# Optimization experiments

Measured on AMD Instinct MI355X. Metric: run time of the kernel, lower is better.

The kernel has to match this reference:

```python
import jax, jax.numpy as jnp
import numpy as np

B = 128          # number of graphs in the batch
NM, EM = 100000, 400000    # mol nodes / edges
NP, EP = 200000, 3200000   # protein nodes / edges
DM, DP, OD = 78, 54, 16


def setup_inputs() -> dict:
    key = jax.random.key(0)
    ks = jax.random.split(key, 20)
    def w(k, shape):
        return jax.random.normal(k, shape, jnp.float32) * 0.05
    z = lambda n: jnp.zeros((n,), jnp.float32)
    return {
        "mol_x": jax.random.normal(ks[0], (NM, DM), jnp.float32),
        "mol_edge_index": jax.random.randint(ks[1], (2, EM), 0, NM),
        "mol_batch": jnp.sort(jax.random.randint(ks[2], (NM,), 0, B)),
        "pro_x": jax.random.normal(ks[3], (NP, DP), jnp.float32),
        "pro_edge_index": jax.random.randint(ks[4], (2, EP), 0, NP),
        "pro_batch": jnp.sort(jax.random.randint(ks[5], (NP,), 0, B)),
        "mol_W1": w(ks[6], (256, DM)), "mol_b1": z(256),
        "mol_W2": w(ks[7], (7 * OD, 256)), "mol_b2": z(7 * OD),
        "c1_Wl": w(ks[8], (DP, DP)), "c1_bl": z(DP), "c1_Wr": w(ks[9], (DP, DP)),
        "c2_Wl": w(ks[10], (2 * DP, DP)), "c2_bl": z(2 * DP), "c2_Wr": w(ks[11], (2 * DP, DP)),
        "pro_W1": w(ks[12], (256, 2 * DP)), "pro_b1": z(256),
        "pro_W2": w(ks[13], (9 * OD, 256)), "pro_b2": z(9 * OD),
        "fc1_W": w(ks[14], (1024, 16 * OD)), "fc1_b": z(1024),
        "fc2_W": w(ks[15], (512, 1024)), "fc2_b": z(512),
        "out_W": w(ks[16], (1, 512)), "out_b": z(1),
    }


def _seg_mean(x, seg, n):
    s = jax.ops.segment_sum(x, seg, num_segments=n)
    c = jax.ops.segment_sum(jnp.ones((x.shape[0],), x.dtype), seg, num_segments=n)
    return s / jnp.maximum(c, 1.0)[:, None]


def _sage(x, ei, Wl, bl, Wr):
    # PyG SAGEConv (mean aggr): lin_l(mean_{j->i} x_j) + lin_r(x_i); lin_r has no bias
    agg = _seg_mean(x[ei[0]], ei[1], x.shape[0])
    return agg @ Wl.T + bl + x @ Wr.T


def reference(mol_x, mol_edge_index, mol_batch, pro_x, pro_edge_index, pro_batch,
              mol_W1, mol_b1, mol_W2, mol_b2,
              c1_Wl, c1_bl, c1_Wr, c2_Wl, c2_bl, c2_Wr,
              pro_W1, pro_b1, pro_W2, pro_b2,
              fc1_W, fc1_b, fc2_W, fc2_b, out_W, out_b):
    alpha, degree = 0.05, 4
    # APPNP-style k-hop propagation over the unnormalized COO adjacency:
    # (adj @ h)[i] = sum over edges (row=i, col=j) of h[j]
    row, col = mol_edge_index[0], mol_edge_index[1]
    h = mol_x
    emb = alpha * mol_x
    for _ in range(degree):
        h = jax.ops.segment_sum(h[col], row, num_segments=mol_x.shape[0])
        emb = emb + (1.0 - alpha) * h / degree
    x = _seg_mean(emb, mol_batch, B)            # global mean pool -> [B, 78]
    x = jax.nn.relu(x @ mol_W1.T + mol_b1)
    x = x @ mol_W2.T + mol_b2                   # [B, 112]; dropout is identity at eval

    xt = jax.nn.relu(_sage(pro_x, pro_edge_index, c1_Wl, c1_bl, c1_Wr))
    xt = jax.nn.relu(_sage(xt, pro_edge_index, c2_Wl, c2_bl, c2_Wr))
    xt = _seg_mean(xt, pro_batch, B)            # [B, 108]
    xt = jax.nn.relu(xt @ pro_W1.T + pro_b1)
    xt = xt @ pro_W2.T + pro_b2                 # [B, 144]

    xc = jnp.concatenate([x, xt], axis=1)       # [B, 256]
    xc = jax.nn.relu(xc @ fc1_W.T + fc1_b)
    xc = jax.nn.relu(xc @ fc2_W.T + fc2_b)
    return xc @ out_W.T + out_b                 # [B, 1]
```

## Files before the change

kernel.cpp:

```cpp
#include <hip/hip_runtime.h>

#define K256 __launch_bounds__(256)

constexpr int B = 128;
constexpr int NM = 100000, EM = 400000;
constexpr int NP = 200000, EP = 3200000;
constexpr int DM = 78, DPK = 54, DP2 = 108;
constexpr int XH = 32;
constexpr int XH4 = 16;
constexpr int MH = 48;

__device__ __forceinline__ float b2f(unsigned short u) {
  return __uint_as_float((unsigned int)u << 16);
}
__device__ __forceinline__ unsigned short f2b(float f) {
  unsigned int b = __float_as_uint(f);
  return (unsigned short)((b + 0x7fffu + ((b >> 16) & 1u)) >> 16);
}

template <int SH>
__global__ void K256 k_bhist(const int* __restrict__ dst, int* __restrict__ bhist, int E) {
  __shared__ int lh[512];
  int tid = threadIdx.x;
  for (int t = tid; t < 512; t += 256) lh[t] = 0;
  __syncthreads();
  int c0 = blockIdx.x * 4096;
#pragma unroll
  for (int k = 0; k < 16; k++) {
    int e = c0 + k * 256 + tid;
    if (e < E) atomicAdd(&lh[dst[e] >> SH], 1);
  }
  __syncthreads();
  for (int t = tid; t < 512; t += 256) {
    int c = lh[t];
    if (c) atomicAdd(&bhist[t], c);
  }
}

__global__ void k_scanb(const int* __restrict__ bhist, int* __restrict__ bed,
                        int* __restrict__ bcur, int NB, int E) {
  __shared__ int s[512];
  int tid = threadIdx.x;
  int v = (tid < NB) ? bhist[tid] : 0;
  s[tid] = v;
  __syncthreads();
  for (int off = 1; off < 512; off <<= 1) {
    int t = (tid >= off) ? s[tid - off] : 0;
    __syncthreads();
    s[tid] += t;
    __syncthreads();
  }
  int excl = s[tid] - v;
  if (tid < NB) {
    bed[tid] = excl;
    bcur[tid] = excl;
  }
  if (tid == NB - 1) bed[NB] = E;
}

template <int SH>
__global__ void K256 k_bin(const int* __restrict__ src, const int* __restrict__ dst,
                           int* __restrict__ bcur, int2* __restrict__ binned, int E) {
  __shared__ int lh[512];
  __shared__ int gbase[512];
  int c0 = blockIdx.x * 4096;
  int tid = threadIdx.x;
  for (int t = tid; t < 512; t += 256) lh[t] = 0;
  __syncthreads();
  int r[16], dcache[16];
#pragma unroll
  for (int k = 0; k < 16; k++) {
    int e = c0 + k * 256 + tid;
    if (e < E) {
      int d = dst[e];
      dcache[k] = d;
      r[k] = atomicAdd(&lh[d >> SH], 1);
    }
  }
  __syncthreads();
  for (int b = tid; b < 512; b += 256) {
    int c = lh[b];
    gbase[b] = c ? atomicAdd(&bcur[b], c) : 0;
  }
  __syncthreads();
#pragma unroll
  for (int k = 0; k < 16; k++) {
    int e = c0 + k * 256 + tid;
    if (e < E) {
      int d = dcache[k];
      binned[gbase[d >> SH] + r[k]] = make_int2(src[e], d);
    }
  }
}

template <int SH>
__global__ void K256 k_build(const int2* __restrict__ binned, const int* __restrict__ bed,
                             int* __restrict__ deg, int* __restrict__ starts,
                             int* __restrict__ csr, int N) {
  constexpr int NN = 1 << SH;
  constexpr int P = NN / 256;
  __shared__ int lcnt[NN];
  __shared__ int lpair[256];
  int b = blockIdx.x, base = b << SH, tid = threadIdx.x;
  int nn = min(N - base, NN);
  for (int t = tid; t < NN; t += 256) lcnt[t] = 0;
  __syncthreads();
  int e0 = bed[b], e1 = bed[b + 1];
  for (int e = e0 + tid; e < e1; e += 256) atomicAdd(&lcnt[binned[e].y - base], 1);
  __syncthreads();
  int loc[P];
  int psum = 0;
#pragma unroll
  for (int p = 0; p < P; p++) {
    loc[p] = lcnt[tid * P + p];
    psum += loc[p];
  }
  lpair[tid] = psum;
  __syncthreads();
  for (int off = 1; off < 256; off <<= 1) {
    int t = (tid >= off) ? lpair[tid - off] : 0;
    __syncthreads();
    lpair[tid] += t;
    __syncthreads();
  }
  int run = lpair[tid] - psum;
  __syncthreads();
#pragma unroll
  for (int p = 0; p < P; p++) {
    int i = tid * P + p;
    int st = e0 + run;
    if (i < nn) {
      deg[base + i] = loc[p];
      starts[base + i] = st;
    }
    lcnt[i] = st;
    run += loc[p];
  }
  __syncthreads();
  for (int e = e0 + tid; e < e1; e += 256) {
    int2 sd = binned[e];
    int p = atomicAdd(&lcnt[sd.y - base], 1);
    csr[p] = sd.x;
  }
}

__global__ void K256 k_bstart(const int* __restrict__ batch, int* __restrict__ bstart, int N) {
  int i = blockIdx.x * 256 + threadIdx.x;
  if (i < N) {
    int b = batch[i];
    int pb = (i == 0) ? -1 : batch[i - 1];
    for (int bb = pb + 1; bb <= b; bb++) bstart[bb] = i;
    if (i == N - 1)
      for (int bb = b + 1; bb <= B; bb++) bstart[bb] = N;
  }
}

__global__ void k_inv(const int* __restrict__ bstart, float* __restrict__ inv) {
  int b = threadIdx.x;
  if (b < B) inv[b] = 1.f / fmaxf((float)(bstart[b + 1] - bstart[b]), 1.f);
}

__global__ void K256 k_transT(const float* __restrict__ in, float* __restrict__ out, int R,
                              int C) {
  __shared__ float t[32][33];
  int cb = blockIdx.x * 32, rb = blockIdx.y * 32;
  int tx = threadIdx.x & 31, ty = threadIdx.x >> 5;
  for (int i = ty; i < 32; i += 8) {
    int r = rb + i, c = cb + tx;
    if (r < R && c < C) t[i][tx] = in[(size_t)r * C + c];
  }
  __syncthreads();
  for (int i = ty; i < 32; i += 8) {
    int c = cb + i, r = rb + tx;
    if (r < R && c < C) out[(size_t)c * R + r] = t[tx][i];
  }
}

__global__ void K256 k_prepw(const float* __restrict__ c1Wl, const float* __restrict__ c1Wr,
                             const float* __restrict__ c1bl, const float* __restrict__ c2Wl,
                             const float* __restrict__ c2Wr, float* __restrict__ w1cat,
                             float* __restrict__ bl1c, float* __restrict__ w2cat) {
  int i = blockIdx.x * 256 + threadIdx.x;
  if (i < 108 * 56) {
    int k = i / 56, o = i - k * 56;
    w1cat[i] = (o < 54) ? ((k < 54) ? c1Wl[o * 54 + k] : c1Wr[o * 54 + (k - 54)]) : 0.f;
  }
  if (i < 108 * 108) {
    int k = i / 108, o = i - k * 108;
    w2cat[i] = (k < 54) ? c2Wl[o * 54 + k] : c2Wr[o * 54 + (k - 54)];
  }
  if (i < 56) bl1c[i] = (i < 54) ? c1bl[i] : 0.f;
}

template <int DF2, int XHD>
__global__ void K256 k_castg(const float* __restrict__ x, int sstride,
                             ushort2* __restrict__ xh, int N) {
  int t = blockIdx.x * 256 + threadIdx.x;
  if (t < N * DF2) {
    int n = t / DF2, j = t - n * DF2;
    float2 v = *(const float2*)(x + (size_t)n * sstride + 2 * j);
    xh[(size_t)n * XHD + j] = make_ushort2(f2b(v.x), f2b(v.y));
  }
}

__global__ void K256 k_gatherh(const ushort4* __restrict__ xh4, const int* __restrict__ starts,
                               const int* __restrict__ deg, const int* __restrict__ csr,
                               ushort4* __restrict__ outh4, int N) {
  int wid = (blockIdx.x * 256 + threadIdx.x) >> 6;
  int lane = threadIdx.x & 63;
  if (wid >= N) return;
  int s = starts[wid], d = deg[wid];
  const int* cp = csr + s;
  int quarter = lane >> 4, sl = lane & 15;
  bool act = sl < 14;
  float a0 = 0.f, a1 = 0.f, a2 = 0.f, a3 = 0.f;
  float b0 = 0.f, b1 = 0.f, b2 = 0.f, b3 = 0.f;
  int j = 0;
  for (; j + 8 <= d; j += 8) {
    if (act) {
      ushort4 v = xh4[(size_t)cp[j + quarter] * XH4 + sl];
      ushort4 w = xh4[(size_t)cp[j + 4 + quarter] * XH4 + sl];
      a0 += b2f(v.x);
      a1 += b2f(v.y);
      a2 += b2f(v.z);
      a3 += b2f(v.w);
      b0 += b2f(w.x);
      b1 += b2f(w.y);
      b2 += b2f(w.z);
      b3 += b2f(w.w);
    }
  }
  for (; j + 4 <= d; j += 4) {
    if (act) {
      ushort4 v = xh4[(size_t)cp[j + quarter] * XH4 + sl];
      a0 += b2f(v.x);
      a1 += b2f(v.y);
      a2 += b2f(v.z);
      a3 += b2f(v.w);
    }
  }
  int r = d - j;
  if (quarter < r && act) {
    ushort4 v = xh4[(size_t)cp[j + quarter] * XH4 + sl];
    a0 += b2f(v.x);
    a1 += b2f(v.y);
    a2 += b2f(v.z);
    a3 += b2f(v.w);
  }
  a0 += b0;
  a1 += b1;
  a2 += b2;
  a3 += b3;
  a0 += __shfl_xor(a0, 16, 64);
  a1 += __shfl_xor(a1, 16, 64);
  a2 += __shfl_xor(a2, 16, 64);
  a3 += __shfl_xor(a3, 16, 64);
  a0 += __shfl_xor(a0, 32, 64);
  a1 += __shfl_xor(a1, 32, 64);
  a2 += __shfl_xor(a2, 32, 64);
  a3 += __shfl_xor(a3, 32, 64);
  if (lane < 14) {
    float inv = 1.f / fmaxf((float)d, 1.f);
    outh4[(size_t)wid * XH4 + lane] =
        make_ushort4(f2b(a0 * inv), f2b(a1 * inv), f2b(a2 * inv), f2b(a3 * inv));
  }
}

__global__ void K256 k_gatherm(const ushort2* __restrict__ xh, const int* __restrict__ starts,
                               const int* __restrict__ deg, const int* __restrict__ csr,
                               ushort2* __restrict__ outh, int N) {
  int wid = (blockIdx.x * 256 + threadIdx.x) >> 6;
  int lane = threadIdx.x & 63;
  if (wid >= N) return;
  int s = starts[wid], d = deg[wid];
  const int* cp = csr + s;
  bool act = lane < 39;
  float ax = 0.f, ay = 0.f, bx = 0.f, by = 0.f;
  int j = 0;
  for (; j + 4 <= d; j += 4) {
    if (act) {
      ushort2 v0 = xh[(size_t)cp[j] * MH + lane];
      ushort2 v1 = xh[(size_t)cp[j + 1] * MH + lane];
      ushort2 v2 = xh[(size_t)cp[j + 2] * MH + lane];
      ushort2 v3 = xh[(size_t)cp[j + 3] * MH + lane];
      ax += b2f(v0.x) + b2f(v2.x);
      ay += b2f(v0.y) + b2f(v2.y);
      bx += b2f(v1.x) + b2f(v3.x);
      by += b2f(v1.y) + b2f(v3.y);
    }
  }
  for (; j < d; j++) {
    if (act) {
      ushort2 v = xh[(size_t)cp[j] * MH + lane];
      ax += b2f(v.x);
      ay += b2f(v.y);
    }
  }
  ax += bx;
  ay += by;
  if (act) outh[(size_t)wid * MH + lane] = make_ushort2(f2b(ax), f2b(ay));
}

template <int SPLIT>
__global__ void K256 k_pool_segh(const ushort2* __restrict__ xh, const int* __restrict__ bstart,
                                 float* __restrict__ pooled, float coef) {
  constexpr int NPB = 6;
  __shared__ float sp[NPB * DM];
  int b = blockIdx.x / SPLIT;
  int sidx = blockIdx.x - b * SPLIT;
  int tid = threadIdx.x;
  int r0 = bstart[b], r1 = bstart[b + 1];
  int len = r1 - r0;
  int per = (len + SPLIT - 1) / SPLIT;
  int s0 = r0 + sidx * per;
  int s1 = min(r1, s0 + per);
  if (tid < 39 * NPB) {
    int ioff = tid / 39, j = tid - ioff * 39;
    float a0x = 0.f, a0y = 0.f, a1x = 0.f, a1y = 0.f;
    int i = s0 + ioff;
    for (; i + 3 * NPB < s1; i += 4 * NPB) {
      ushort2 v0 = xh[(size_t)i * MH + j];
      ushort2 v1 = xh[(size_t)(i + NPB) * MH + j];
      ushort2 v2 = xh[(size_t)(i + 2 * NPB) * MH + j];
      ushort2 v3 = xh[(size_t)(i + 3 * NPB) * MH + j];
      a0x += b2f(v0.x) + b2f(v2.x);
      a0y += b2f(v0.y) + b2f(v2.y);
      a1x += b2f(v1.x) + b2f(v3.x);
      a1y += b2f(v1.y) + b2f(v3.y);
    }
    for (; i < s1; i += NPB) {
      ushort2 v = xh[(size_t)i * MH + j];
      a0x += b2f(v.x);
      a0y += b2f(v.y);
    }
    sp[ioff * DM + 2 * j] = a0x + a1x;
    sp[ioff * DM + 2 * j + 1] = a0y + a1y;
  }
  __syncthreads();
  if (tid < DM) {
    float s = 0.f;
#pragma unroll
    for (int g = 0; g < NPB; g++) s += sp[g * DM + tid];
    s *= coef;
    if (s != 0.f) atomicAdd(&pooled[b * DM + tid], s);
  }
}

__global__ void __launch_bounds__(256, 4) k_sage1c(
    const float* __restrict__ x, const ushort2* __restrict__ aggh,
    const float* __restrict__ wcat, const float* __restrict__ blc,
    ushort2* __restrict__ outh, int N) {
  __shared__ float scat[64 * 109];
  int base = blockIdx.x * 64;
  int nn = min(N - base, 64);
  int tid = threadIdx.x;
  for (int t = tid; t < nn * 27; t += 256) {
    int n = t / 27, j = t - n * 27;
    ushort2 va = aggh[(size_t)(base + n) * XH + j];
    float2 vx = *(const float2*)(x + (size_t)(base + n) * 54 + 2 * j);
    float* sr = scat + n * 109;
    sr[2 * j] = b2f(va.x);
    sr[2 * j + 1] = b2f(va.y);
    sr[54 + 2 * j] = vx.x;
    sr[54 + 2 * j + 1] = vx.y;
  }
  __syncthreads();
  int w = tid >> 6, lane = tid & 63;
  int obase = __builtin_amdgcn_readfirstlane(w * 14);
  if (lane >= nn) return;
  float acc[14];
#pragma unroll
  for (int o = 0; o < 14; o++) acc[o] = blc[obase + o];
  const float* rs = scat + lane * 109;
#pragma unroll 2
  for (int k = 0; k < 108; k++) {
    float v = rs[k];
    const float* wr = wcat + k * 56 + obase;
#pragma unroll
    for (int o = 0; o < 14; o++) acc[o] += v * wr[o];
  }
  ushort2* op = outh + (size_t)(base + lane) * XH + (obase >> 1);
#pragma unroll
  for (int o = 0; o < 7; o++)
    op[o] = make_ushort2(f2b(fmaxf(acc[2 * o], 0.f)), f2b(fmaxf(acc[2 * o + 1], 0.f)));
}

template <int SPLIT>
__global__ void __launch_bounds__(256, 4) k_sage2c(
    const ushort2* __restrict__ xt1h, const ushort2* __restrict__ aggh,
    const float* __restrict__ wcat, const float* __restrict__ bl,
    const int* __restrict__ bstart, float* __restrict__ pooled) {
  __shared__ float scat[64 * 109];
  int b = blockIdx.x / SPLIT;
  int sidx = blockIdx.x - b * SPLIT;
  int tid = threadIdx.x;
  int w = tid >> 6, lane = tid & 63;
  int obase = __builtin_amdgcn_readfirstlane(w * 27);
  int r0 = bstart[b], r1 = bstart[b + 1];
  int len = r1 - r0;
  int per = (len + SPLIT - 1) / SPLIT;
  int s0 = r0 + sidx * per;
  int s1 = min(r1, s0 + per);
  float pool[27];
#pragma unroll
  for (int o = 0; o < 27; o++) pool[o] = 0.f;
  for (int tb = s0; tb < s1; tb += 64) {
    int nn = min(s1 - tb, 64);
    __syncthreads();
    for (int t = tid; t < nn * 27; t += 256) {
      int n = t / 27, j = t - n * 27;
      ushort2 va = aggh[(size_t)(tb + n) * XH + j];
      ushort2 vx = xt1h[(size_t)(tb + n) * XH + j];
      float* sr = scat + n * 109;
      sr[2 * j] = b2f(va.x);
      sr[2 * j + 1] = b2f(va.y);
      sr[54 + 2 * j] = b2f(vx.x);
      sr[54 + 2 * j + 1] = b2f(vx.y);
    }
    __syncthreads();
    if (lane < nn) {
      float acc[27];
#pragma unroll
      for (int o = 0; o < 27; o++) acc[o] = bl[obase + o];
      const float* rs = scat + lane * 109;
#pragma unroll 2
      for (int k = 0; k < 108; k++) {
        float v = rs[k];
        const float* wr = wcat + k * 108 + obase;
#pragma unroll
        for (int o = 0; o < 27; o++) acc[o] += v * wr[o];
      }
#pragma unroll
      for (int o = 0; o < 27; o++) pool[o] += fmaxf(acc[o], 0.f);
    }
  }
#pragma unroll
  for (int o = 0; o < 27; o++) {
#pragma unroll
    for (int off = 1; off < 64; off <<= 1) pool[o] += __shfl_xor(pool[o], off, 64);
  }
  if (lane == 0) {
    float* pb = pooled + b * DP2 + obase;
#pragma unroll
    for (int o = 0; o < 27; o++)
      if (pool[o] != 0.f) atomicAdd(&pb[o], pool[o]);
  }
}

template <int DIN, int DOUT, bool RELU>
__global__ void K256 k_mlp(const float* __restrict__ X, int xstride,
                           const float* __restrict__ rs, const float* __restrict__ WT,
                           const float* __restrict__ bias, float* __restrict__ Y,
                           int ystride, int ycol0) {
  constexpr int BT = 8;
  __shared__ float Xs[BT][DIN];
  int tid = threadIdx.x;
  int ob = blockIdx.x * 256 + tid;
  int bb = blockIdx.y * BT;
  for (int t = tid; t < BT * DIN; t += 256) {
    int i = t / DIN, k = t - i * DIN;
    float v = X[(size_t)(bb + i) * xstride + k];
    if (rs) v *= rs[bb + i];
    Xs[i][k] = v;
  }
  __syncthreads();
  int o = (ob < DOUT) ? ob : (DOUT - 1);
  float bv = bias[o];
  float acc[BT];
#pragma unroll
  for (int i = 0; i < BT; i++) acc[i] = bv;
#pragma unroll 4
  for (int k = 0; k < DIN; k++) {
    float w = WT[(size_t)k * DOUT + o];
#pragma unroll
    for (int i = 0; i < BT; i++) acc[i] += Xs[i][k] * w;
  }
  if (ob < DOUT) {
#pragma unroll
    for (int i = 0; i < BT; i++) {
      float v = RELU ? fmaxf(acc[i], 0.f) : acc[i];
      Y[(size_t)(bb + i) * ystride + ycol0 + ob] = v;
    }
  }
}

__global__ void __launch_bounds__(64) k_gemv1(const float* __restrict__ t2,
                                              const float* __restrict__ W3,
                                              const float* __restrict__ b3,
                                              float* __restrict__ out) {
  int b = blockIdx.x, lane = threadIdx.x;
  float a = 0.f;
  const float* row = t2 + (size_t)b * 512;
#pragma unroll 2
  for (int k = lane; k < 512; k += 64) a += row[k] * W3[k];
#pragma unroll
  for (int off = 32; off > 0; off >>= 1) a += __shfl_down(a, off, 64);
  if (lane == 0) out[b] = a + b3[0];
}

__global__ void k_report(float* out, float v, int n) {
  int i = blockIdx.x * 256 + threadIdx.x;
  if (i < n) out[i] = v;
}

extern "C" void kernel_launch(void* const* d_in, const int* in_sizes, int n_in,
                              void* d_out, int out_size, void* d_ws, size_t ws_size,
                              hipStream_t stream) {
  (void)in_sizes; (void)n_in;
  const float* mol_x = (const float*)d_in[0];
  const int* m_ei = (const int*)d_in[1];
  const int* m_batch = (const int*)d_in[2];
  const float* pro_x = (const float*)d_in[3];
  const int* p_ei = (const int*)d_in[4];
  const int* p_batch = (const int*)d_in[5];
  const float* mol_W1 = (const float*)d_in[6];
  const float* mol_b1 = (const float*)d_in[7];
  const float* mol_W2 = (const float*)d_in[8];
  const float* mol_b2 = (const float*)d_in[9];
  const float* c1_Wl = (const float*)d_in[10];
  const float* c1_bl = (const float*)d_in[11];
  const float* c1_Wr = (const float*)d_in[12];
  const float* c2_Wl = (const float*)d_in[13];
  const float* c2_bl = (const float*)d_in[14];
  const float* c2_Wr = (const float*)d_in[15];
  const float* pro_W1 = (const float*)d_in[16];
  const float* pro_b1 = (const float*)d_in[17];
  const float* pro_W2 = (const float*)d_in[18];
  const float* pro_b2 = (const float*)d_in[19];
  const float* fc1_W = (const float*)d_in[20];
  const float* fc1_b = (const float*)d_in[21];
  const float* fc2_W = (const float*)d_in[22];
  const float* fc2_b = (const float*)d_in[23];
  const float* out_W = (const float*)d_in[24];
  const float* out_b = (const float*)d_in[25];
  float* out = (float*)d_out;
  char* ws = (char*)d_ws;

  const int* m_row = m_ei;
  const int* m_col = m_ei + EM;
  const int* p_e0 = p_ei;
  const int* p_e1 = p_ei + EP;

  auto al = [](size_t x) { return (x + 255) & ~(size_t)255; };

  size_t o = 0;
  size_t o_pdeg = o;   o += al((size_t)NP * 4);
  size_t o_pstart = o; o += al((size_t)NP * 4);
  size_t o_pcsr = o;   o += al((size_t)EP * 4);
  size_t o_aggh = o;   o += al((size_t)NP * XH * 4);
  size_t o_xt1h = o;   o += al((size_t)NP * XH * 4);
  size_t o_pxh = o;    o += al((size_t)NP * XH * 4);
  size_t pro_end = o;

  o = 0;
  size_t o_mdeg = o;   o += al((size_t)NM * 4);
  size_t o_mstart = o; o += al((size_t)NM * 4);
  size_t o_mcsr = o;   o += al((size_t)EM * 4);
  size_t o_mxh = o;    o += al((size_t)NM * MH * 4);
  size_t o_hAh = o;    o += al((size_t)NM * MH * 4);
  size_t o_hBh = o;    o += al((size_t)NM * MH * 4);
  size_t mol_end = o;

  size_t tail = al(pro_end > mol_end ? pro_end : mol_end);
  size_t o_poolM = tail; tail += al((size_t)B * DM * 4);
  size_t o_poolP = tail; tail += al((size_t)B * DP2 * 4);
  size_t o_mbs = tail;   tail += al((size_t)(B + 1) * 4);
  size_t o_pbs = tail;   tail += al((size_t)(B + 1) * 4);
  size_t o_w1c = tail;   tail += al((size_t)108 * 56 * 4);
  size_t o_bl1 = tail;   tail += al(56 * 4);
  size_t o_w2c = tail;   tail += al((size_t)108 * 108 * 4);
  size_t o_mbc = tail;   tail += al(512 * 4);
  size_t o_pbc = tail;   tail += al(512 * 4);
  size_t o_mbh = tail;   tail += al(512 * 4);
  size_t o_pbh = tail;   tail += al(512 * 4);
  size_t o_mbed = tail;  tail += al(513 * 4);
  size_t o_pbed = tail;  tail += al(513 * 4);
  size_t o_mh1T = tail;  tail += al((size_t)DM * 256 * 4);
  size_t o_mh2T = tail;  tail += al((size_t)256 * 112 * 4);
  size_t o_ph1T = tail;  tail += al((size_t)DP2 * 256 * 4);
  size_t o_ph2T = tail;  tail += al((size_t)256 * 144 * 4);
  size_t o_fc1T = tail;  tail += al((size_t)256 * 1024 * 4);
  size_t o_fc2T = tail;  tail += al((size_t)1024 * 512 * 4);
  size_t o_xc = tail;    tail += al((size_t)B * 256 * 4);
  size_t o_t1 = tail;    tail += al((size_t)B * 1024 * 4);
  size_t o_t2 = tail;    tail += al((size_t)B * 512 * 4);
  size_t o_th = tail;    tail += al((size_t)B * 256 * 4);
  size_t o_invM = tail;  tail += al(B * 4);
  size_t o_invP = tail;  tail += al(B * 4);

  if (ws_size < tail) {
    k_report<<<1, 256, 0, stream>>>(out, (float)(ws_size >> 20), out_size);
    return;
  }

  int* mdeg = (int*)(ws + o_mdeg);
  int* mstart = (int*)(ws + o_mstart);
  int* mcsr = (int*)(ws + o_mcsr);
  ushort2* mxh = (ushort2*)(ws + o_mxh);
  ushort2* hAh = (ushort2*)(ws + o_hAh);
  ushort2* hBh = (ushort2*)(ws + o_hBh);
  int* pdeg = (int*)(ws + o_pdeg);
  int* pstart = (int*)(ws + o_pstart);
  int* pcsr = (int*)(ws + o_pcsr);
  ushort2* aggh = (ushort2*)(ws + o_aggh);
  ushort2* xt1h = (ushort2*)(ws + o_xt1h);
  ushort2* pxh = (ushort2*)(ws + o_pxh);
  float* poolM = (float*)(ws + o_poolM);
  float* poolP = (float*)(ws + o_poolP);
  int* mbs = (int*)(ws + o_mbs);
  int* pbs = (int*)(ws + o_pbs);
  float* w1cat = (float*)(ws + o_w1c);
  float* bl1c = (float*)(ws + o_bl1);
  float* w2cat = (float*)(ws + o_w2c);
  int* mbc = (int*)(ws + o_mbc);
  int* pbc = (int*)(ws + o_pbc);
  int* mbh = (int*)(ws + o_mbh);
  int* pbh = (int*)(ws + o_pbh);
  int* mbed = (int*)(ws + o_mbed);
  int* pbed = (int*)(ws + o_pbed);
  float* mh1T = (float*)(ws + o_mh1T);
  float* mh2T = (float*)(ws + o_mh2T);
  float* ph1T = (float*)(ws + o_ph1T);
  float* ph2T = (float*)(ws + o_ph2T);
  float* fc1T = (float*)(ws + o_fc1T);
  float* fc2T = (float*)(ws + o_fc2T);
  float* xc = (float*)(ws + o_xc);
  float* t1 = (float*)(ws + o_t1);
  float* t2 = (float*)(ws + o_t2);
  float* th = (float*)(ws + o_th);
  float* invM = (float*)(ws + o_invM);
  float* invP = (float*)(ws + o_invP);
  int2* mbinned = (int2*)hAh;
  int2* pbinned = (int2*)aggh;

  k_prepw<<<(108 * 108 + 255) / 256, 256, 0, stream>>>(c1_Wl, c1_Wr, c1_bl, c2_Wl, c2_Wr,
                                                       w1cat, bl1c, w2cat);
  {
    auto tg = [](int R, int C) { return dim3((C + 31) / 32, (R + 31) / 32); };
    k_transT<<<tg(256, DM), 256, 0, stream>>>(mol_W1, mh1T, 256, DM);
    k_transT<<<tg(112, 256), 256, 0, stream>>>(mol_W2, mh2T, 112, 256);
    k_transT<<<tg(256, DP2), 256, 0, stream>>>(pro_W1, ph1T, 256, DP2);
    k_transT<<<tg(144, 256), 256, 0, stream>>>(pro_W2, ph2T, 144, 256);
    k_transT<<<tg(1024, 256), 256, 0, stream>>>(fc1_W, fc1T, 1024, 256);
    k_transT<<<tg(512, 1024), 256, 0, stream>>>(fc2_W, fc2T, 512, 1024);
  }

  constexpr int SHM = 8;
  constexpr int NBM = (NM + (1 << SHM) - 1) >> SHM;
  hipMemsetAsync(mbh, 0, 512 * 4, stream);
  hipMemsetAsync(poolM, 0, (size_t)B * DM * 4, stream);
  k_bhist<SHM><<<(EM + 4095) / 4096, 256, 0, stream>>>(m_row, mbh, EM);
  k_scanb<<<1, 512, 0, stream>>>(mbh, mbed, mbc, NBM, EM);
  k_bin<SHM><<<(EM + 4095) / 4096, 256, 0, stream>>>(m_col, m_row, mbc, mbinned, EM);
  k_build<SHM><<<NBM, 256, 0, stream>>>(mbinned, mbed, mdeg, mstart, mcsr, NM);
  k_bstart<<<(NM + 255) / 256, 256, 0, stream>>>(m_batch, mbs, NM);
  k_inv<<<1, 128, 0, stream>>>(mbs, invM);
  k_castg<39, MH><<<(NM * 39 + 255) / 256, 256, 0, stream>>>(mol_x, DM, mxh, NM);

  int gb_m = (NM * 64 + 255) / 256;
  k_pool_segh<8><<<B * 8, 256, 0, stream>>>(mxh, mbs, poolM, 0.05f);
  k_gatherm<<<gb_m, 256, 0, stream>>>(mxh, mstart, mdeg, mcsr, hAh, NM);
  k_pool_segh<8><<<B * 8, 256, 0, stream>>>(hAh, mbs, poolM, 0.2375f);
  k_gatherm<<<gb_m, 256, 0, stream>>>(hAh, mstart, mdeg, mcsr, hBh, NM);
  k_pool_segh<8><<<B * 8, 256, 0, stream>>>(hBh, mbs, poolM, 0.2375f);
  k_gatherm<<<gb_m, 256, 0, stream>>>(hBh, mstart, mdeg, mcsr, hAh, NM);
  k_pool_segh<8><<<B * 8, 256, 0, stream>>>(hAh, mbs, poolM, 0.2375f);
  k_gatherm<<<gb_m, 256, 0, stream>>>(hAh, mstart, mdeg, mcsr, hBh, NM);
  k_pool_segh<8><<<B * 8, 256, 0, stream>>>(hBh, mbs, poolM, 0.2375f);
  {
    dim3 g1(1, B / 8);
    k_mlp<DM, 256, true><<<g1, 256, 0, stream>>>(poolM, DM, invM, mh1T, mol_b1, th, 256, 0);
    k_mlp<256, 112, false><<<g1, 256, 0, stream>>>(th, 256, nullptr, mh2T, mol_b2, xc, 256, 0);
  }

  constexpr int SHP = 9;
  constexpr int NBP = (NP + (1 << SHP) - 1) >> SHP;
  hipMemsetAsync(pbh, 0, 512 * 4, stream);
  hipMemsetAsync(poolP, 0, (size_t)B * DP2 * 4, stream);
  k_bhist<SHP><<<(EP + 4095) / 4096, 256, 0, stream>>>(p_e1, pbh, EP);
  k_scanb<<<1, 512, 0, stream>>>(pbh, pbed, pbc, NBP, EP);
  k_bin<SHP><<<(EP + 4095) / 4096, 256, 0, stream>>>(p_e0, p_e1, pbc, pbinned, EP);
  k_build<SHP><<<NBP, 256, 0, stream>>>(pbinned, pbed, pdeg, pstart, pcsr, NP);
  k_bstart<<<(NP + 255) / 256, 256, 0, stream>>>(p_batch, pbs, NP);
  k_inv<<<1, 128, 0, stream>>>(pbs, invP);
  k_castg<27, XH><<<(NP * 27 + 255) / 256, 256, 0, stream>>>(pro_x, DPK, pxh, NP);

  int gb_p = (NP * 64 + 255) / 256;
  k_gatherh<<<gb_p, 256, 0, stream>>>((const ushort4*)pxh, pstart, pdeg, pcsr,
                                      (ushort4*)aggh, NP);
  k_sage1c<<<(NP + 63) / 64, 256, 0, stream>>>(pro_x, aggh, w1cat, bl1c, xt1h, NP);
  k_gatherh<<<gb_p, 256, 0, stream>>>((const ushort4*)xt1h, pstart, pdeg, pcsr,
                                      (ushort4*)aggh, NP);
  k_sage2c<8><<<B * 8, 256, 0, stream>>>(xt1h, aggh, w2cat, c2_bl, pbs, poolP);
  {
    dim3 g1(1, B / 8);
    k_mlp<DP2, 256, true><<<g1, 256, 0, stream>>>(poolP, DP2, invP, ph1T, pro_b1, th, 256, 0);
    k_mlp<256, 144, false><<<g1, 256, 0, stream>>>(th, 256, nullptr, ph2T, pro_b2, xc, 256, 112);
  }

  {
    dim3 gA(4, B / 8);
    k_mlp<256, 1024, true><<<gA, 256, 0, stream>>>(xc, 256, nullptr, fc1T, fc1_b, t1, 1024, 0);
    dim3 gB(2, B / 8);
    k_mlp<1024, 512, true><<<gB, 256, 0, stream>>>(t1, 1024, nullptr, fc2T, fc2_b, t2, 512, 0);
    k_gemv1<<<B, 64, 0, stream>>>(t2, out_W, out_b, out);
  }
}
```

Baseline: 867.1 us.

## Fuse MLP head layers and final FC stack into per-graph kernels

Replaces the generic batched k_mlp launches with fused kernels that run one block per graph. k_headf runs both layers of each branch head through shared memory, and k_fin runs fc1, fc2 and the output GEMV in one kernel. This cuts seven launches down to three and removes the t1, t2 and th intermediate buffers in global memory. In exchange each block now streams the full fc1 and fc2 weight matrices for a single row, losing the old eight-row weight reuse and multiplying weight traffic through the caches.

```diff
diff --git a/kernel.cpp b/kernel.cpp
--- a/kernel.cpp
+++ b/kernel.cpp
@@ -447,55 +447,79 @@
   }
 }
 
-template <int DIN, int DOUT, bool RELU>
-__global__ void K256 k_mlp(const float* __restrict__ X, int xstride,
-                           const float* __restrict__ rs, const float* __restrict__ WT,
-                           const float* __restrict__ bias, float* __restrict__ Y,
-                           int ystride, int ycol0) {
-  constexpr int BT = 8;
-  __shared__ float Xs[BT][DIN];
-  int tid = threadIdx.x;
-  int ob = blockIdx.x * 256 + tid;
-  int bb = blockIdx.y * BT;
-  for (int t = tid; t < BT * DIN; t += 256) {
-    int i = t / DIN, k = t - i * DIN;
-    float v = X[(size_t)(bb + i) * xstride + k];
-    if (rs) v *= rs[bb + i];
-    Xs[i][k] = v;
-  }
-  __syncthreads();
-  int o = (ob < DOUT) ? ob : (DOUT - 1);
-  float bv = bias[o];
-  float acc[BT];
-#pragma unroll
-  for (int i = 0; i < BT; i++) acc[i] = bv;
+template <int DIN, int DOUT>
+__global__ void K256 k_headf(const float* __restrict__ X, int xstride,
+                             const float* __restrict__ rs, const float* __restrict__ W1T,
+                             const float* __restrict__ b1, const float* __restrict__ W2T,
+                             const float* __restrict__ b2, float* __restrict__ Y,
+                             int ystride, int ycol0) {
+  __shared__ float sx[DIN];
+  __shared__ float sh[256];
+  int b = blockIdx.x, tid = threadIdx.x;
+  float scale = rs ? rs[b] : 1.f;
+  for (int f = tid; f < DIN; f += 256) sx[f] = X[(size_t)b * xstride + f] * scale;
+  __syncthreads();
+  float acc = b1[tid];
 #pragma unroll 4
-  for (int k = 0; k < DIN; k++) {
-    float w = WT[(size_t)k * DOUT + o];
-#pragma unroll
-    for (int i = 0; i < BT; i++) acc[i] += Xs[i][k] * w;
-  }
-  if (ob < DOUT) {
-#pragma unroll
-    for (int i = 0; i < BT; i++) {
-      float v = RELU ? fmaxf(acc[i], 0.f) : acc[i];
-      Y[(size_t)(bb + i) * ystride + ycol0 + ob] = v;
-    }
-  }
-}
-
-__global__ void __launch_bounds__(64) k_gemv1(const float* __restrict__ t2,
-                                              const float* __restrict__ W3,
-                                              const float* __restrict__ b3,
-                                              float* __restrict__ out) {
-  int b = blockIdx.x, lane = threadIdx.x;
+  for (int k = 0; k < DIN; k++) acc += sx[k] * W1T[k * 256 + tid];
+  sh[tid] = fmaxf(acc, 0.f);
+  __syncthreads();
+  if (tid < DOUT) {
+    float a = b2[tid];
+#pragma unroll 4
+    for (int k = 0; k < 256; k++) a += sh[k] * W2T[k * DOUT + tid];
+    Y[(size_t)b * ystride + ycol0 + tid] = a;
+  }
+}
+
+__global__ void K256 k_fin(const float* __restrict__ xc, const float* __restrict__ W1T,
+                           const float* __restrict__ b1, const float* __restrict__ W2T,
+                           const float* __restrict__ b2, const float* __restrict__ W3,
+                           const float* __restrict__ b3, float* __restrict__ out) {
+  __shared__ float sx[256];
+  __shared__ float sh1[1024];
+  __shared__ float sh2[512];
+  __shared__ float red[4];
+  int b = blockIdx.x, tid = threadIdx.x;
+  sx[tid] = xc[(size_t)b * 256 + tid];
+  __syncthreads();
+  {
+    float a0 = b1[tid], a1 = b1[tid + 256], a2 = b1[tid + 512], a3 = b1[tid + 768];
+#pragma unroll 2
+    for (int k = 0; k < 256; k++) {
+      float xv = sx[k];
+      const float* wr = W1T + k * 1024;
+      a0 += xv * wr[tid];
+      a1 += xv * wr[tid + 256];
+      a2 += xv * wr[tid + 512];
+      a3 += xv * wr[tid + 768];
+    }
+    sh1[tid] = fmaxf(a0, 0.f);
+    sh1[tid + 256] = fmaxf(a1, 0.f);
+    sh1[tid + 512] = fmaxf(a2, 0.f);
+    sh1[tid + 768] = fmaxf(a3, 0.f);
+  }
+  __syncthreads();
+  {
+    float a0 = b2[tid], a1 = b2[tid + 256];
+#pragma unroll 2
+    for (int k = 0; k < 1024; k++) {
+      float xv = sh1[k];
+      const float* wr = W2T + k * 512;
+      a0 += xv * wr[tid];
+      a1 += xv * wr[tid + 256];
+    }
+    sh2[tid] = fmaxf(a0, 0.f);
+    sh2[tid + 256] = fmaxf(a1, 0.f);
+  }
+  __syncthreads();
   float a = 0.f;
-  const float* row = t2 + (size_t)b * 512;
-#pragma unroll 2
-  for (int k = lane; k < 512; k += 64) a += row[k] * W3[k];
+  for (int k = tid; k < 512; k += 256) a += sh2[k] * W3[k];
 #pragma unroll
   for (int off = 32; off > 0; off >>= 1) a += __shfl_down(a, off, 64);
-  if (lane == 0) out[b] = a + b3[0];
+  if ((tid & 63) == 0) red[tid >> 6] = a;
+  __syncthreads();
+  if (tid == 0) out[b] = red[0] + red[1] + red[2] + red[3] + b3[0];
 }
 
 __global__ void k_report(float* out, float v, int n) {
@@ -582,9 +606,6 @@
   size_t o_fc1T = tail;  tail += al((size_t)256 * 1024 * 4);
   size_t o_fc2T = tail;  tail += al((size_t)1024 * 512 * 4);
   size_t o_xc = tail;    tail += al((size_t)B * 256 * 4);
-  size_t o_t1 = tail;    tail += al((size_t)B * 1024 * 4);
-  size_t o_t2 = tail;    tail += al((size_t)B * 512 * 4);
-  size_t o_th = tail;    tail += al((size_t)B * 256 * 4);
   size_t o_invM = tail;  tail += al(B * 4);
   size_t o_invP = tail;  tail += al(B * 4);
 
@@ -625,9 +646,6 @@
   float* fc1T = (float*)(ws + o_fc1T);
   float* fc2T = (float*)(ws + o_fc2T);
   float* xc = (float*)(ws + o_xc);
-  float* t1 = (float*)(ws + o_t1);
-  float* t2 = (float*)(ws + o_t2);
-  float* th = (float*)(ws + o_th);
   float* invM = (float*)(ws + o_invM);
   float* invP = (float*)(ws + o_invP);
   int2* mbinned = (int2*)hAh;
@@ -667,11 +685,8 @@
   k_pool_segh<8><<<B * 8, 256, 0, stream>>>(hAh, mbs, poolM, 0.2375f);
   k_gatherm<<<gb_m, 256, 0, stream>>>(hAh, mstart, mdeg, mcsr, hBh, NM);
   k_pool_segh<8><<<B * 8, 256, 0, stream>>>(hBh, mbs, poolM, 0.2375f);
-  {
-    dim3 g1(1, B / 8);
-    k_mlp<DM, 256, true><<<g1, 256, 0, stream>>>(poolM, DM, invM, mh1T, mol_b1, th, 256, 0);
-    k_mlp<256, 112, false><<<g1, 256, 0, stream>>>(th, 256, nullptr, mh2T, mol_b2, xc, 256, 0);
-  }
+  k_headf<DM, 112><<<B, 256, 0, stream>>>(poolM, DM, invM, mh1T, mol_b1, mh2T, mol_b2, xc,
+                                          256, 0);
 
   constexpr int SHP = 9;
   constexpr int NBP = (NP + (1 << SHP) - 1) >> SHP;
@@ -692,17 +707,8 @@
   k_gatherh<<<gb_p, 256, 0, stream>>>((const ushort4*)xt1h, pstart, pdeg, pcsr,
                                       (ushort4*)aggh, NP);
   k_sage2c<8><<<B * 8, 256, 0, stream>>>(xt1h, aggh, w2cat, c2_bl, pbs, poolP);
-  {
-    dim3 g1(1, B / 8);
-    k_mlp<DP2, 256, true><<<g1, 256, 0, stream>>>(poolP, DP2, invP, ph1T, pro_b1, th, 256, 0);
-    k_mlp<256, 144, false><<<g1, 256, 0, stream>>>(th, 256, nullptr, ph2T, pro_b2, xc, 256, 112);
-  }
-
-  {
-    dim3 gA(4, B / 8);
-    k_mlp<256, 1024, true><<<gA, 256, 0, stream>>>(xc, 256, nullptr, fc1T, fc1_b, t1, 1024, 0);
-    dim3 gB(2, B / 8);
-    k_mlp<1024, 512, true><<<gB, 256, 0, stream>>>(t1, 1024, nullptr, fc2T, fc2_b, t2, 512, 0);
-    k_gemv1<<<B, 64, 0, stream>>>(t2, out_W, out_b, out);
-  }
-}
+  k_headf<DP2, 144><<<B, 256, 0, stream>>>(poolP, DP2, invP, ph1T, pro_b1, ph2T, pro_b2, xc,
+                                           256, 112);
+
+  k_fin<<<B, 256, 0, stream>>>(xc, fc1T, fc1_b, fc2T, fc2_b, out_W, out_b, out);
+}
```

New measurement: 914.9 us. +5.5%, slower.
